# Kernel optimization log

Measured on AMD Instinct MI355X. Metric: run time of the kernel, lower is better.

Reference implementation:

```python
import jax, jax.numpy as jnp
import numpy as np

KAPPA = 0.99
A_RHO = 1.0

def project_norm_inf(W, v):
    """Project each row of W onto the l1-ball of radius v (=> ||W||_inf <= v).
    Rows whose abs-sum already <= v are left untouched (as in the source)."""
    def proj_row(a):
        abs_a = jnp.abs(a)
        s = jnp.sum(abs_a)
        u = jnp.sort(abs_a)[::-1]                      # descending
        css = jnp.cumsum(u) - v
        k = jnp.arange(1, a.shape[0] + 1, dtype=a.dtype)
        rho = jnp.sum((u - css / k) > 0)               # number of active coords
        theta = css[rho - 1] / rho.astype(a.dtype)
        proj = jnp.sign(a) * jnp.maximum(abs_a - theta, 0.0)
        return jnp.where(s > v, proj, a)
    return jax.vmap(proj_row)(W)

def setup_inputs() -> dict:
    m, p, n = 32, 64, 10000
    key = jax.random.key(0)
    ks = jax.random.split(key, 5)
    stdv = 1.0 / np.sqrt(m)  # matches init(): uniform(-1/sqrt(m), 1/sqrt(m))
    W = jax.random.uniform(ks[0], (m, m), minval=-stdv, maxval=stdv, dtype=jnp.float32)
    Omega_1 = jax.random.uniform(ks[1], (m, p), minval=-stdv, maxval=stdv, dtype=jnp.float32)
    Omega_2 = jax.random.uniform(ks[2], (m, p), minval=-stdv, maxval=stdv, dtype=jnp.float32)
    X_0 = jnp.zeros((m, n), dtype=jnp.float32)
    A_raw = jax.random.uniform(ks[3], (n, n), dtype=jnp.float32)
    A = A_raw / jnp.sum(A_raw, axis=0, keepdims=True)  # column-stochastic => rho(A) <= 1
    U = jax.random.normal(ks[4], (p, n), dtype=jnp.float32)
    return {"W": W, "Omega_1": Omega_1, "Omega_2": Omega_2,
            "X_0": X_0, "A": A, "U": U, "fw_mitr": 30}

def reference(W, Omega_1, Omega_2, X_0, A, U, fw_mitr):
    # W <- projection onto ||W||_inf <= kappa / A_rho (contraction guarantee)
    Wp = project_norm_inf(W, KAPPA / A_RHO)
    # support_1 = ((U^T @ Omega_1^T)^T) then ((A^T @ .^T)^T)  ==  Omega_1 @ U @ A
    b_Omega = (Omega_1 @ U) @ A                       # [m, n]
    _support_2 = Omega_2 @ U                          # computed but unused, as in source
    # ImplicitFunction forward: Picard iteration X <- phi(W X A + b), phi = ReLU
    def step(X, _):
        X_new = jax.nn.relu((Wp @ X) @ A + b_Omega)
        return X_new, None
    X, _ = jax.lax.scan(step, X_0, None, length=fw_mitr)
    return X
```

## Files before the change

kernel.cpp:

```cpp
#include <hip/hip_runtime.h>


#define N      10000
#define M      32
#define PDIM   64
#define ITERS  30
#define KAPPA  0.99f
#define KP     10240
#define NSTEP  (KP / 32)
#define KSPLIT 16
#define SPW    (NSTEP / KSPLIT)
#define NT     625
#define NQ     157

typedef short  s16x8 __attribute__((ext_vector_type(8)));
typedef __bf16 b16x8 __attribute__((ext_vector_type(8)));
typedef float  f32x4 __attribute__((ext_vector_type(4)));

template <typename V>
__device__ __forceinline__ auto mfma_sel(V a, V b, f32x4 c, int)
    -> decltype(__builtin_amdgcn_mfma_f32_16x16x32_bf16(a, b, c, 0, 0, 0)) {
  return __builtin_amdgcn_mfma_f32_16x16x32_bf16(a, b, c, 0, 0, 0);
}
template <typename V>
__device__ __forceinline__ f32x4 mfma_sel(V a, V b, f32x4 c, long) {
  b16x8 a2 = __builtin_bit_cast(b16x8, a);
  b16x8 b2 = __builtin_bit_cast(b16x8, b);
  return __builtin_amdgcn_mfma_f32_16x16x32_bf16(a2, b2, c, 0, 0, 0);
}
__device__ __forceinline__ f32x4 MFMA_BF16(s16x8 a, s16x8 b, f32x4 c) {
  return mfma_sel(a, b, c, 0);
}

__device__ __forceinline__ short f2bf(float f) {
  union { float f; unsigned u; } v; v.f = f;
  unsigned r = v.u + 0x7fffu + ((v.u >> 16) & 1u);
  return (short)(r >> 16);
}
__device__ __forceinline__ float bf2f(short h) {
  union { unsigned u; float f; } v; v.u = ((unsigned)(unsigned short)h) << 16;
  return v.f;
}

__global__ void proj_w_kernel(const float* __restrict__ W, float* __restrict__ Wp) {
  int r = threadIdx.x;
  if (r >= M) return;
  float a[M], u[M];
  float s = 0.f;
  for (int c = 0; c < M; ++c) { a[c] = W[r * M + c]; u[c] = fabsf(a[c]); s += u[c]; }
  for (int i = 1; i < M; ++i) {
    float key = u[i]; int t = i - 1;
    while (t >= 0 && u[t] < key) { u[t + 1] = u[t]; --t; }
    u[t + 1] = key;
  }
  const float v = KAPPA;
  float csum = 0.f, theta = 0.f;
  for (int i = 0; i < M; ++i) {
    csum += u[i];
    float cs = csum - v;
    if (u[i] - cs / (float)(i + 1) > 0.f) theta = cs / (float)(i + 1);
  }
  for (int c = 0; c < M; ++c) {
    float pa = fmaxf(fabsf(a[c]) - theta, 0.f);
    pa = (a[c] > 0.f) ? pa : ((a[c] < 0.f) ? -pa : 0.f);
    Wp[r * M + c] = (s > v) ? pa : a[c];
  }
}

__global__ void compute_c_kernel(const float* __restrict__ O1, const float* __restrict__ U,
                                 float* __restrict__ Ct) {
  __shared__ float o1[M * PDIM];
  int tid = threadIdx.x;
  for (int t = tid; t < M * PDIM; t += 128) o1[t] = O1[t];
  __syncthreads();
  int j = blockIdx.x * 128 + tid;
  if (j >= N) return;
  float u[PDIM];
  #pragma unroll
  for (int l = 0; l < PDIM; ++l) u[l] = U[(size_t)l * N + j];
  for (int i = 0; i < M; ++i) {
    float s = 0.f;
    #pragma unroll
    for (int l = 0; l < PDIM; ++l) s += o1[i * PDIM + l] * u[l];
    Ct[(size_t)j * M + i] = s;
  }
}


__global__ __launch_bounds__(256) void pack_b_kernel(const float* __restrict__ A,
                                                     short* __restrict__ Bp) {
  __shared__ float t[128][17];
  const int tid = threadIdx.x;
  const int j0 = blockIdx.x * 16, k0 = blockIdx.y * 128;
  const int jj = tid & 15, kk = tid >> 4;
  for (int r = 0; r < 8; ++r) {
    int k = k0 + kk + r * 16;
    float v = 0.f;
    if (k < N) v = A[(size_t)k * N + (j0 + jj)];
    t[kk + r * 16][jj] = v;
  }
  __syncthreads();
  const int sl = tid >> 6, lane = tid & 63;
  const int jcol = lane & 15, ko = (lane >> 4) * 8;
  short out[8];
  #pragma unroll
  for (int e = 0; e < 8; ++e) out[e] = f2bf(t[sl * 32 + ko + e][jcol]);
  size_t dst = (((size_t)blockIdx.x * NSTEP + (size_t)blockIdx.y * 4 + sl) * 64 + lane) * 8;
  *(s16x8*)(Bp + dst) = *(const s16x8*)out;
}


__global__ __launch_bounds__(128) void compute_y0_kernel(const float* __restrict__ X0,
    const float* __restrict__ Wp, const float* __restrict__ Ct, short* __restrict__ Yp) {
  __shared__ float w[M * M];
  __shared__ short ly[4 * 4 * 512];
  int tid = threadIdx.x;
  for (int t = tid; t < M * M; t += 128) w[t] = Wp[t];
  __syncthreads();
  const int j = blockIdx.x * 128 + tid;
  const int s_local = tid >> 5;
  const int laneoff = ((tid >> 3) & 3) << 4;
  const int e = tid & 7;
  float y[M];
  if (j < N) {
    float x[M];
    #pragma unroll
    for (int i = 0; i < M; ++i) x[i] = X0[(size_t)i * N + j];
    for (int i = 0; i < M; ++i) {
      float s = Ct[(size_t)j * M + i];
      #pragma unroll
      for (int l = 0; l < M; ++l) s += w[i * M + l] * x[l];
      y[i] = s;
    }
  } else {
    #pragma unroll
    for (int i = 0; i < M; ++i) y[i] = 0.f;
  }
  #pragma unroll
  for (int i = 0; i < M; ++i) {
    short h = f2bf(y[i]);
    short l2 = f2bf(y[i] - bf2f(h));
    int ph_h = (i >> 4) * 2, base = s_local * 512 + ((i & 15) + laneoff) * 8 + e;
    ly[ph_h * 2048 + base] = h;
    ly[(ph_h + 1) * 2048 + base] = l2;
  }
  __syncthreads();
  const int sbase = blockIdx.x * 4;
  for (int c = tid; c < 1024; c += 128) {
    int ph = c >> 8, rem = c & 255;
    int sl = rem >> 6, off = (rem & 63) * 8;
    size_t dst = ((size_t)ph * NSTEP + sbase + sl) * 512 + off;
    *(s16x8*)(Yp + dst) = *(const s16x8*)(ly + ph * 2048 + sl * 512 + off);
  }
}

__global__ __launch_bounds__(256) void mfma_gemm_kernel(const short* __restrict__ Yp,
    const short* __restrict__ Bp, float* __restrict__ P) {
  const int lane = threadIdx.x & 63;
  const int wid  = threadIdx.x >> 6;
  const int tq   = blockIdx.x * 4 + wid;
  if (tq >= NQ) return;
  const int t0 = tq * 4;
  const int nt = (NT - t0 < 4) ? (NT - t0) : 4;
  const int s0 = blockIdx.y * SPW;
  const size_t lo = (size_t)lane * 8;

  const short* yp0 = Yp + ((size_t)0 * NSTEP + s0) * 512 + lo;
  const short* yp1 = Yp + ((size_t)1 * NSTEP + s0) * 512 + lo;
  const short* yp2 = Yp + ((size_t)2 * NSTEP + s0) * 512 + lo;
  const short* yp3 = Yp + ((size_t)3 * NSTEP + s0) * 512 + lo;
  const short* bp0 = Bp + ((size_t)(t0 + 0) * NSTEP + s0) * 512 + lo;
  const short* bp1 = Bp + ((size_t)((t0 + 1 < NT) ? t0 + 1 : NT - 1) * NSTEP + s0) * 512 + lo;
  const short* bp2 = Bp + ((size_t)((t0 + 2 < NT) ? t0 + 2 : NT - 1) * NSTEP + s0) * 512 + lo;
  const short* bp3 = Bp + ((size_t)((t0 + 3 < NT) ? t0 + 3 : NT - 1) * NSTEP + s0) * 512 + lo;

  f32x4 a00 = {0.f, 0.f, 0.f, 0.f};
  f32x4 a01 = a00, a10 = a00, a11 = a00, a20 = a00, a21 = a00, a30 = a00, a31 = a00;

  #pragma unroll 2
  for (int s = 0; s < SPW; ++s) {
    const size_t so = (size_t)s * 512;
    s16x8 yh0 = *(const s16x8*)(yp0 + so);
    s16x8 yl0 = *(const s16x8*)(yp1 + so);
    s16x8 yh1 = *(const s16x8*)(yp2 + so);
    s16x8 yl1 = *(const s16x8*)(yp3 + so);
    s16x8 b0  = *(const s16x8*)(bp0 + so);
    s16x8 b1  = *(const s16x8*)(bp1 + so);
    s16x8 b2  = *(const s16x8*)(bp2 + so);
    s16x8 b3  = *(const s16x8*)(bp3 + so);
    a00 = MFMA_BF16(yh0, b0, a00);  a00 = MFMA_BF16(yl0, b0, a00);
    a01 = MFMA_BF16(yh1, b0, a01);  a01 = MFMA_BF16(yl1, b0, a01);
    a10 = MFMA_BF16(yh0, b1, a10);  a10 = MFMA_BF16(yl0, b1, a10);
    a11 = MFMA_BF16(yh1, b1, a11);  a11 = MFMA_BF16(yl1, b1, a11);
    a20 = MFMA_BF16(yh0, b2, a20);  a20 = MFMA_BF16(yl0, b2, a20);
    a21 = MFMA_BF16(yh1, b2, a21);  a21 = MFMA_BF16(yl1, b2, a21);
    a30 = MFMA_BF16(yh0, b3, a30);  a30 = MFMA_BF16(yl0, b3, a30);
    a31 = MFMA_BF16(yh1, b3, a31);  a31 = MFMA_BF16(yl1, b3, a31);
  }

  float* pbase = P + (size_t)blockIdx.y * (size_t)(M * N);
  const int jcol = lane & 15, i0 = (lane >> 4) * 4;
  f32x4 acc0[4] = {a00, a10, a20, a30};
  f32x4 acc1[4] = {a01, a11, a21, a31};
  #pragma unroll
  for (int tt = 0; tt < 4; ++tt) {
    if (tt >= nt) break;
    float* p = pbase + (size_t)(t0 + tt) * 16 + jcol;
    #pragma unroll
    for (int r = 0; r < 4; ++r) {
      p[(size_t)(i0 + r) * N]      = acc0[tt][r];
      p[(size_t)(i0 + 16 + r) * N] = acc1[tt][r];
    }
  }
}

__global__ __launch_bounds__(128) void fused_reduce_kernel(const float* __restrict__ P_,
    const float* __restrict__ Wp, const float* __restrict__ Ct, float* __restrict__ X,
    short* __restrict__ Yp) {
  __shared__ float w[M * M];
  __shared__ short ly[4 * 4 * 512];
  int tid = threadIdx.x;
  for (int t = tid; t < M * M; t += 128) w[t] = Wp[t];
  __syncthreads();
  const int j = blockIdx.x * 128 + tid;
  const int s_local = tid >> 5;
  const int laneoff = ((tid >> 3) & 3) << 4;
  const int e = tid & 7;
  float y[M];
  if (j < N) {
    float x[M];
    #pragma unroll
    for (int i = 0; i < M; ++i) x[i] = 0.f;
    for (int s = 0; s < KSPLIT; ++s) {
      #pragma unroll
      for (int i = 0; i < M; ++i) x[i] += P_[((size_t)s * M + i) * N + j];
    }
    #pragma unroll
    for (int i = 0; i < M; ++i) { x[i] = fmaxf(x[i], 0.f); X[(size_t)i * N + j] = x[i]; }
    for (int i = 0; i < M; ++i) {
      float s = Ct[(size_t)j * M + i];
      #pragma unroll
      for (int l = 0; l < M; ++l) s += w[i * M + l] * x[l];
      y[i] = s;
    }
  } else {
    #pragma unroll
    for (int i = 0; i < M; ++i) y[i] = 0.f;
  }
  #pragma unroll
  for (int i = 0; i < M; ++i) {
    short h = f2bf(y[i]);
    short l2 = f2bf(y[i] - bf2f(h));
    int ph_h = (i >> 4) * 2, base = s_local * 512 + ((i & 15) + laneoff) * 8 + e;
    ly[ph_h * 2048 + base] = h;
    ly[(ph_h + 1) * 2048 + base] = l2;
  }
  __syncthreads();
  const int sbase = blockIdx.x * 4;
  for (int c = tid; c < 1024; c += 128) {
    int ph = c >> 8, rem = c & 255;
    int sl = rem >> 6, off = (rem & 63) * 8;
    size_t dst = ((size_t)ph * NSTEP + sbase + sl) * 512 + off;
    *(s16x8*)(Yp + dst) = *(const s16x8*)(ly + ph * 2048 + sl * 512 + off);
  }
}


__global__ void compute_y0_f32(const float* __restrict__ X0, const float* __restrict__ Wp,
                               const float* __restrict__ Ct, float* __restrict__ Yt) {
  __shared__ float w[M * M];
  int tid = threadIdx.x;
  for (int t = tid; t < M * M; t += 128) w[t] = Wp[t];
  __syncthreads();
  int j = blockIdx.x * 128 + tid;
  if (j >= N) return;
  float x[M];
  #pragma unroll
  for (int i = 0; i < M; ++i) x[i] = X0[(size_t)i * N + j];
  for (int i = 0; i < M; ++i) {
    float s = Ct[(size_t)j * M + i];
    #pragma unroll
    for (int l = 0; l < M; ++l) s += w[i * M + l] * x[l];
    Yt[(size_t)j * M + i] = s;
  }
}

__global__ __launch_bounds__(256) void gemm_f32(const float* __restrict__ Yt,
                                                const float* __restrict__ A,
                                                float* __restrict__ P, int krange) {
  const int tid = threadIdx.x;
  const int j = blockIdx.x * 512 + tid * 2;
  const bool inb = (j < N);
  const int k0 = blockIdx.y * krange;

  float2 acc[M];
  #pragma unroll
  for (int i = 0; i < M; ++i) acc[i] = float2{0.f, 0.f};

  const float* arow = A + (size_t)k0 * N + j;
  const float4* yrow = (const float4*)(Yt + (size_t)k0 * M);

  #pragma unroll 2
  for (int k = 0; k < krange; ++k) {
    float2 a = float2{0.f, 0.f};
    if (inb) a = *(const float2*)(arow + (size_t)k * N);
    #pragma unroll
    for (int q = 0; q < 8; ++q) {
      float4 y = yrow[k * 8 + q];
      acc[4 * q + 0].x += y.x * a.x;  acc[4 * q + 0].y += y.x * a.y;
      acc[4 * q + 1].x += y.y * a.x;  acc[4 * q + 1].y += y.y * a.y;
      acc[4 * q + 2].x += y.z * a.x;  acc[4 * q + 2].y += y.z * a.y;
      acc[4 * q + 3].x += y.w * a.x;  acc[4 * q + 3].y += y.w * a.y;
    }
  }

  if (inb) {
    float* p = P + (size_t)blockIdx.y * M * N + j;
    #pragma unroll
    for (int i = 0; i < M; ++i) *(float2*)(p + (size_t)i * N) = acc[i];
  }
}

__global__ void fused_reduce_f32(const float* __restrict__ P_, const float* __restrict__ Wp,
                                 const float* __restrict__ Ct, float* __restrict__ X,
                                 float* __restrict__ Yt, int ksplit) {
  __shared__ float w[M * M];
  int tid = threadIdx.x;
  for (int t = tid; t < M * M; t += 128) w[t] = Wp[t];
  __syncthreads();
  int j = blockIdx.x * 128 + tid;
  if (j >= N) return;
  float x[M];
  #pragma unroll
  for (int i = 0; i < M; ++i) x[i] = 0.f;
  for (int s = 0; s < ksplit; ++s) {
    #pragma unroll
    for (int i = 0; i < M; ++i) x[i] += P_[((size_t)s * M + i) * N + j];
  }
  #pragma unroll
  for (int i = 0; i < M; ++i) { x[i] = fmaxf(x[i], 0.f); X[(size_t)i * N + j] = x[i]; }
  for (int i = 0; i < M; ++i) {
    float s = Ct[(size_t)j * M + i];
    #pragma unroll
    for (int l = 0; l < M; ++l) s += w[i * M + l] * x[l];
    Yt[(size_t)j * M + i] = s;
  }
}

extern "C" void kernel_launch(void* const* d_in, const int* in_sizes, int n_in,
                              void* d_out, int out_size, void* d_ws, size_t ws_size,
                              hipStream_t stream) {
  const float* W  = (const float*)d_in[0];
  const float* O1 = (const float*)d_in[1];
  const float* X0 = (const float*)d_in[3];
  const float* A  = (const float*)d_in[4];
  const float* U  = (const float*)d_in[5];
  float* Xout = (float*)d_out;

  const int jb = (N + 127) / 128;

  const size_t need_bf16 = 4096
                         + (size_t)N * M * 4
                         + (size_t)4 * NSTEP * 512 * 2
                         + (size_t)KSPLIT * M * N * 4
                         + (size_t)NT * NSTEP * 512 * 2;

  if (ws_size >= need_bf16) {
    float* Wp = (float*)d_ws;
    float* Ct = Wp + 1024;
    short* Yp = (short*)(Ct + (size_t)N * M);
    float* P  = (float*)(Yp + (size_t)4 * NSTEP * 512);
    short* Bp = (short*)(P + (size_t)KSPLIT * M * N);

    proj_w_kernel<<<1, 64, 0, stream>>>(W, Wp);
    compute_c_kernel<<<jb, 128, 0, stream>>>(O1, U, Ct);
    pack_b_kernel<<<dim3(NT, KP / 128), 256, 0, stream>>>(A, Bp);
    compute_y0_kernel<<<KP / 128, 128, 0, stream>>>(X0, Wp, Ct, Yp);
    for (int it = 0; it < ITERS; ++it) {
      mfma_gemm_kernel<<<dim3((NQ + 3) / 4, KSPLIT), 256, 0, stream>>>(Yp, Bp, P);
      fused_reduce_kernel<<<jb, 128, 0, stream>>>(P, Wp, Ct, Xout, Yp);
    }
  } else {
    auto bytes_needed = [](int ks) {
      return (size_t)(1024 + 2 * (size_t)N * M + (size_t)ks * M * N) * 4;
    };
    const int ksplit = (ws_size >= bytes_needed(50)) ? 50 : 25;
    const int krange = N / ksplit;
    const int jtiles = (N + 511) / 512;

    float* Wp = (float*)d_ws;
    float* Ct = Wp + 1024;
    float* Yt = Ct + (size_t)N * M;
    float* P  = Yt + (size_t)N * M;

    proj_w_kernel<<<1, 64, 0, stream>>>(W, Wp);
    compute_c_kernel<<<jb, 128, 0, stream>>>(O1, U, Ct);
    compute_y0_f32<<<jb, 128, 0, stream>>>(X0, Wp, Ct, Yt);
    for (int it = 0; it < ITERS; ++it) {
      gemm_f32<<<dim3(jtiles, ksplit), 256, 0, stream>>>(Yt, A, P, krange);
      fused_reduce_f32<<<jb, 128, 0, stream>>>(P, Wp, Ct, Xout, Yt, ksplit);
    }
  }
}
```

Baseline: 2.469 ms.

## Halve GEMM tiles per wave and split reduce across four wave groups

The MFMA GEMM now gives each wave two 16-column output tiles instead of four. That doubles the grid to 79x16 blocks for more occupancy and parallelism, at the cost of re-reading the Y operand twice as often. The reduce kernel now handles 64 columns per 256-thread block. Each wave group sums four of the K-split partials, the groups combine through shared memory, and each thread then computes 8 of the 32 W·x rows. This cuts per-thread serial loads and register pressure but adds shared-memory traffic and extra barriers.

```diff
diff --git a/kernel.cpp b/kernel.cpp
--- a/kernel.cpp
+++ b/kernel.cpp
@@ -11,7 +11,8 @@
 #define KSPLIT 16
 #define SPW    (NSTEP / KSPLIT)
 #define NT     625
-#define NQ     157
+#define NP2    313
+#define GX     79
 
 typedef short  s16x8 __attribute__((ext_vector_type(8)));
 typedef __bf16 b16x8 __attribute__((ext_vector_type(8)));
@@ -109,7 +110,6 @@
   *(s16x8*)(Bp + dst) = *(const s16x8*)out;
 }
 
-
 __global__ __launch_bounds__(128) void compute_y0_kernel(const float* __restrict__ X0,
     const float* __restrict__ Wp, const float* __restrict__ Ct, short* __restrict__ Yp) {
   __shared__ float w[M * M];
@@ -158,10 +158,10 @@
     const short* __restrict__ Bp, float* __restrict__ P) {
   const int lane = threadIdx.x & 63;
   const int wid  = threadIdx.x >> 6;
-  const int tq   = blockIdx.x * 4 + wid;
-  if (tq >= NQ) return;
-  const int t0 = tq * 4;
-  const int nt = (NT - t0 < 4) ? (NT - t0) : 4;
+  const int tp   = blockIdx.x * 4 + wid;
+  if (tp >= NP2) return;
+  const int t0 = tp * 2;
+  const bool has2 = (t0 + 1 < NT);
   const int s0 = blockIdx.y * SPW;
   const size_t lo = (size_t)lane * 8;
 
@@ -169,13 +169,11 @@
   const short* yp1 = Yp + ((size_t)1 * NSTEP + s0) * 512 + lo;
   const short* yp2 = Yp + ((size_t)2 * NSTEP + s0) * 512 + lo;
   const short* yp3 = Yp + ((size_t)3 * NSTEP + s0) * 512 + lo;
-  const short* bp0 = Bp + ((size_t)(t0 + 0) * NSTEP + s0) * 512 + lo;
-  const short* bp1 = Bp + ((size_t)((t0 + 1 < NT) ? t0 + 1 : NT - 1) * NSTEP + s0) * 512 + lo;
-  const short* bp2 = Bp + ((size_t)((t0 + 2 < NT) ? t0 + 2 : NT - 1) * NSTEP + s0) * 512 + lo;
-  const short* bp3 = Bp + ((size_t)((t0 + 3 < NT) ? t0 + 3 : NT - 1) * NSTEP + s0) * 512 + lo;
+  const short* bp0 = Bp + ((size_t)t0 * NSTEP + s0) * 512 + lo;
+  const short* bp1 = Bp + ((size_t)(has2 ? t0 + 1 : t0) * NSTEP + s0) * 512 + lo;
 
   f32x4 a00 = {0.f, 0.f, 0.f, 0.f};
-  f32x4 a01 = a00, a10 = a00, a11 = a00, a20 = a00, a21 = a00, a30 = a00, a31 = a00;
+  f32x4 a01 = a00, a10 = a00, a11 = a00;
 
   #pragma unroll 2
   for (int s = 0; s < SPW; ++s) {
@@ -186,82 +184,98 @@
     s16x8 yl1 = *(const s16x8*)(yp3 + so);
     s16x8 b0  = *(const s16x8*)(bp0 + so);
     s16x8 b1  = *(const s16x8*)(bp1 + so);
-    s16x8 b2  = *(const s16x8*)(bp2 + so);
-    s16x8 b3  = *(const s16x8*)(bp3 + so);
     a00 = MFMA_BF16(yh0, b0, a00);  a00 = MFMA_BF16(yl0, b0, a00);
     a01 = MFMA_BF16(yh1, b0, a01);  a01 = MFMA_BF16(yl1, b0, a01);
     a10 = MFMA_BF16(yh0, b1, a10);  a10 = MFMA_BF16(yl0, b1, a10);
     a11 = MFMA_BF16(yh1, b1, a11);  a11 = MFMA_BF16(yl1, b1, a11);
-    a20 = MFMA_BF16(yh0, b2, a20);  a20 = MFMA_BF16(yl0, b2, a20);
-    a21 = MFMA_BF16(yh1, b2, a21);  a21 = MFMA_BF16(yl1, b2, a21);
-    a30 = MFMA_BF16(yh0, b3, a30);  a30 = MFMA_BF16(yl0, b3, a30);
-    a31 = MFMA_BF16(yh1, b3, a31);  a31 = MFMA_BF16(yl1, b3, a31);
   }
 
   float* pbase = P + (size_t)blockIdx.y * (size_t)(M * N);
   const int jcol = lane & 15, i0 = (lane >> 4) * 4;
-  f32x4 acc0[4] = {a00, a10, a20, a30};
-  f32x4 acc1[4] = {a01, a11, a21, a31};
-  #pragma unroll
-  for (int tt = 0; tt < 4; ++tt) {
-    if (tt >= nt) break;
-    float* p = pbase + (size_t)(t0 + tt) * 16 + jcol;
+  float* p0 = pbase + (size_t)t0 * 16 + jcol;
+  #pragma unroll
+  for (int r = 0; r < 4; ++r) {
+    p0[(size_t)(i0 + r) * N]      = a00[r];
+    p0[(size_t)(i0 + 16 + r) * N] = a01[r];
+  }
+  if (has2) {
+    float* p1 = pbase + (size_t)(t0 + 1) * 16 + jcol;
     #pragma unroll
     for (int r = 0; r < 4; ++r) {
-      p[(size_t)(i0 + r) * N]      = acc0[tt][r];
-      p[(size_t)(i0 + 16 + r) * N] = acc1[tt][r];
-    }
-  }
-}
-
-__global__ __launch_bounds__(128) void fused_reduce_kernel(const float* __restrict__ P_,
+      p1[(size_t)(i0 + r) * N]      = a10[r];
+      p1[(size_t)(i0 + 16 + r) * N] = a11[r];
+    }
+  }
+}
+
+__global__ __launch_bounds__(256) void fused_reduce_kernel(const float* __restrict__ P_,
     const float* __restrict__ Wp, const float* __restrict__ Ct, float* __restrict__ X,
     short* __restrict__ Yp) {
   __shared__ float w[M * M];
-  __shared__ short ly[4 * 4 * 512];
-  int tid = threadIdx.x;
-  for (int t = tid; t < M * M; t += 128) w[t] = Wp[t];
-  __syncthreads();
-  const int j = blockIdx.x * 128 + tid;
-  const int s_local = tid >> 5;
-  const int laneoff = ((tid >> 3) & 3) << 4;
-  const int e = tid & 7;
-  float y[M];
+  __shared__ float xp[4][M][64];
+  __shared__ float xs[M][64];
+  __shared__ short ly[4 * 2 * 512];
+  const int tid = threadIdx.x;
+  for (int t = tid; t < M * M; t += 256) w[t] = Wp[t];
+  const int jb0 = blockIdx.x * 64;
+  const int jj = tid & 63, q = tid >> 6;
+  const int j = jb0 + jj;
+
+  float part[M];
+  #pragma unroll
+  for (int i = 0; i < M; ++i) part[i] = 0.f;
   if (j < N) {
-    float x[M];
-    #pragma unroll
-    for (int i = 0; i < M; ++i) x[i] = 0.f;
-    for (int s = 0; s < KSPLIT; ++s) {
+    for (int ss = 0; ss < 4; ++ss) {
+      const int s = q * 4 + ss;
       #pragma unroll
-      for (int i = 0; i < M; ++i) x[i] += P_[((size_t)s * M + i) * N + j];
-    }
-    #pragma unroll
-    for (int i = 0; i < M; ++i) { x[i] = fmaxf(x[i], 0.f); X[(size_t)i * N + j] = x[i]; }
-    for (int i = 0; i < M; ++i) {
+      for (int i = 0; i < M; ++i) part[i] += P_[((size_t)s * M + i) * N + j];
+    }
+  }
+  #pragma unroll
+  for (int i = 0; i < M; ++i) xp[q][i][jj] = part[i];
+  __syncthreads();
+
+  for (int c = tid; c < M * 64; c += 256) {
+    int i = c >> 6, j2 = c & 63;
+    float v = xp[0][i][j2] + xp[1][i][j2] + xp[2][i][j2] + xp[3][i][j2];
+    v = fmaxf(v, 0.f);
+    xs[i][j2] = v;
+    if (jb0 + j2 < N) X[(size_t)i * N + (jb0 + j2)] = v;
+  }
+  __syncthreads();
+
+  float y[8];
+  if (j < N) {
+    #pragma unroll
+    for (int r = 0; r < 8; ++r) {
+      const int i = q * 8 + r;
       float s = Ct[(size_t)j * M + i];
       #pragma unroll
-      for (int l = 0; l < M; ++l) s += w[i * M + l] * x[l];
-      y[i] = s;
+      for (int l = 0; l < M; ++l) s += w[i * M + l] * xs[l][jj];
+      y[r] = s;
     }
   } else {
     #pragma unroll
-    for (int i = 0; i < M; ++i) y[i] = 0.f;
-  }
-  #pragma unroll
-  for (int i = 0; i < M; ++i) {
-    short h = f2bf(y[i]);
-    short l2 = f2bf(y[i] - bf2f(h));
-    int ph_h = (i >> 4) * 2, base = s_local * 512 + ((i & 15) + laneoff) * 8 + e;
-    ly[ph_h * 2048 + base] = h;
-    ly[(ph_h + 1) * 2048 + base] = l2;
-  }
-  __syncthreads();
-  const int sbase = blockIdx.x * 4;
-  for (int c = tid; c < 1024; c += 128) {
-    int ph = c >> 8, rem = c & 255;
-    int sl = rem >> 6, off = (rem & 63) * 8;
-    size_t dst = ((size_t)ph * NSTEP + sbase + sl) * 512 + off;
-    *(s16x8*)(Yp + dst) = *(const s16x8*)(ly + ph * 2048 + sl * 512 + off);
+    for (int r = 0; r < 8; ++r) y[r] = 0.f;
+  }
+  const int sl = jj >> 5, laneoff = ((jj >> 3) & 3) << 4, e = jj & 7;
+  #pragma unroll
+  for (int r = 0; r < 8; ++r) {
+    const int i = q * 8 + r;
+    short h = f2bf(y[r]);
+    short l2 = f2bf(y[r] - bf2f(h));
+    int ph_h = (i >> 4) * 2, base = sl * 512 + ((i & 15) + laneoff) * 8 + e;
+    ly[ph_h * 1024 + base] = h;
+    ly[(ph_h + 1) * 1024 + base] = l2;
+  }
+  __syncthreads();
+
+  const int sbase = blockIdx.x * 2;
+  for (int c = tid; c < 512; c += 256) {
+    int ph = c >> 7, rem = c & 127;
+    int s2 = rem >> 6, off = (rem & 63) * 8;
+    size_t dst = ((size_t)ph * NSTEP + sbase + s2) * 512 + off;
+    *(s16x8*)(Yp + dst) = *(const s16x8*)(ly + ph * 1024 + s2 * 512 + off);
   }
 }
 
@@ -376,9 +390,10 @@
     compute_c_kernel<<<jb, 128, 0, stream>>>(O1, U, Ct);
     pack_b_kernel<<<dim3(NT, KP / 128), 256, 0, stream>>>(A, Bp);
     compute_y0_kernel<<<KP / 128, 128, 0, stream>>>(X0, Wp, Ct, Yp);
+    const int rb = (N + 63) / 64;
     for (int it = 0; it < ITERS; ++it) {
-      mfma_gemm_kernel<<<dim3((NQ + 3) / 4, KSPLIT), 256, 0, stream>>>(Yp, Bp, P);
-      fused_reduce_kernel<<<jb, 128, 0, stream>>>(P, Wp, Ct, Xout, Yp);
+      mfma_gemm_kernel<<<dim3(GX, KSPLIT), 256, 0, stream>>>(Yp, Bp, P);
+      fused_reduce_kernel<<<rb, 256, 0, stream>>>(P, Wp, Ct, Xout, Yp);
     }
   } else {
     auto bytes_needed = [](int ks) {
```

After: 2.076 ms. 15.9% less time.
